# Performance work log

Hardware: AMD Instinct MI355X
Metric: run time of the kernel (lower is better)

The kernel has to match this reference:

```python
import jax, jax.numpy as jnp
import numpy as np
from functools import partial

# ---- config (scaled-up from repo globals) ----
B, T = 2, 1024          # batch, seq (block_size)
C = 1024                # n_embd
H = 16                  # n_heads
G = 2                   # n_groups -> n_kv_heads = H//G = 8, n_q_heads = G = 2
D = C // H              # d_head = 64
Q = G                   # query linears per head
NHID = 4 * C            # expert hidden (Expert default 4*n_embd)
E = 2                   # n_experts
K = 1                   # top_k_experts
WINDOW = 256            # window_size
EPS = 1e-5


def setup_inputs() -> dict:
    key = jax.random.key(0)
    ks = jax.random.split(key, 20)
    s = 0.02
    f32 = jnp.float32
    return {
        "x": jax.random.normal(ks[0], (B, T, C), f32),
        # attention params (per-head stacked)
        "Wq": jax.random.normal(ks[1], (H, Q, C, D), f32) * s,
        "Wk": jax.random.normal(ks[2], (H, C, D), f32) * s,
        "Wv": jax.random.normal(ks[3], (H, C, D), f32) * s,
        "Wp": jax.random.normal(ks[4], (C, C), f32) * s,
        "bp": jnp.zeros((C,), f32),
        # layernorms
        "ln1_g": jnp.ones((C,), f32), "ln1_b": jnp.zeros((C,), f32),
        "ln2_g": jnp.ones((C,), f32), "ln2_b": jnp.zeros((C,), f32),
        # router gate
        "Wg": jax.random.normal(ks[5], (C, E), f32) * s,
        "bg": jnp.zeros((E,), f32),
        # experts (stacked over E): Linear(C->NHID) -> SwiGLU(NHID) -> Linear(NHID->C)
        "Ew1": jax.random.normal(ks[6], (E, C, NHID), f32) * s,
        "Eb1": jnp.zeros((E, NHID), f32),
        "Ews": jax.random.normal(ks[7], (E, NHID, NHID), f32) * s,
        "Ebs": jnp.zeros((E, NHID), f32),
        "Ebeta": jax.random.normal(ks[8], (E,), f32),
        "Ewg": jax.random.normal(ks[9], (E, NHID, NHID), f32) * s,
        "Ebg": jnp.zeros((E, NHID), f32),
        "Ew2": jax.random.normal(ks[10], (E, NHID, C), f32) * s,
        "Eb2": jnp.zeros((E, C), f32),
    }


def _layer_norm(x, g, b):
    mean = jnp.mean(x, axis=-1, keepdims=True)
    var = jnp.var(x, axis=-1, keepdims=True, ddof=1)  # torch .var() is unbiased
    return (x - mean) / jnp.sqrt(var + EPS) * g + b


def _forward(x, Wq, Wk, Wv, Wp, bp, ln1_g, ln1_b, ln2_g, ln2_b,
             Wg, bg, Ew1, Eb1, Ews, Ebs, Ebeta, Ewg, Ebg, Ew2, Eb2):
    # ---- pre-norm GQA-SWA attention ----
    xn = _layer_norm(x, ln1_g, ln1_b)
    k = jnp.einsum('btc,hcd->hbtd', xn, Wk)          # [H,B,T,D]
    q = jnp.einsum('btc,hqcd->hqbtd', xn, Wq)        # [H,Q,B,T,D]
    v = jnp.einsum('btc,hcd->hbtd', xn, Wv)
    # faithful to torch keys.view(B, C, T): memory reinterpret, NOT transpose
    kr = k.reshape(H, B, D, T)
    scores = jnp.einsum('hqbtd,hbds->hbts', q, kr) * (D ** -0.5)  # sum over Q
    # only the past-window mask is applied (the causal masked_fill is unassigned in source)
    past_mask = jnp.tril(jnp.ones((T, T), jnp.float32), -WINDOW)
    scores = jnp.where(past_mask == 1, -jnp.inf, scores)
    w = jax.nn.softmax(scores, axis=-1)
    o = jnp.einsum('hbts,hbsd->hbtd', w, v)
    o = o.transpose(1, 2, 0, 3).reshape(B, T, C)     # concat heads
    x = x + o @ Wp + bp

    # ---- top-k MoE router ----
    xn2 = _layer_norm(x, ln2_g, ln2_b)
    logits = xn2 @ Wg + bg                           # [B,T,E]
    topw, topi = jax.lax.top_k(logits, K)            # [B,T,K]
    topw = jax.nn.softmax(topw, axis=1)              # faithful bug: softmax over token dim
    # dense expert compute (vectorized replacement for per-expert gather/scatter)
    h1 = jnp.einsum('btc,ech->ebth', xn2, Ew1) + Eb1[:, None, None, :]      # [E,B,T,NHID]
    sx = jnp.einsum('ebth,ehk->ebtk', h1, Ews) + Ebs[:, None, None, :]
    swish = sx * jax.nn.sigmoid(Ebeta[:, None, None, None] * sx)
    glu = jnp.einsum('ebth,ehk->ebtk', h1, Ewg) + Ebg[:, None, None, :]
    eout = jnp.einsum('ebtk,ekc->ebtc', swish * glu, Ew2) + Eb2[:, None, None, :]
    # per-token per-expert mixing weight (top-k indices are distinct)
    onehot = topi[..., None] == jnp.arange(E)        # [B,T,K,E]
    coef = jnp.sum(jnp.where(onehot, topw[..., None], 0.0), axis=2)         # [B,T,E]
    moe = jnp.einsum('bte,ebtc->btc', coef, eout)
    return x + moe


def reference(x, Wq, Wk, Wv, Wp, bp, ln1_g, ln1_b, ln2_g, ln2_b,
              Wg, bg, Ew1, Eb1, Ews, Ebs, Ebeta, Ewg, Ebg, Ew2, Eb2):
    return _forward(x, Wq, Wk, Wv, Wp, bp, ln1_g, ln1_b, ln2_g, ln2_b,
                    Wg, bg, Ew1, Eb1, Ews, Ebs, Ebeta, Ewg, Ebg, Ew2, Eb2)
```

## Files before the change

### kernel.cpp

```cpp
#include <hip/hip_runtime.h>
#include <hip/hip_bf16.h>
#include <cmath>

#define B_    2
#define T_    1024
#define BT_   2048
#define C_    1024
#define H_    16
#define NH_   4096
#define E_    2
#define WIN_  256
#define G_    8

typedef unsigned short u16;
typedef __attribute__((ext_vector_type(8))) short short8;
typedef __attribute__((ext_vector_type(4))) float f32x4;

__device__ __forceinline__ u16 f2b(float f) {
    __hip_bfloat16 h = __float2bfloat16(f);
    return *(u16*)&h;
}
__device__ __forceinline__ float b2f(u16 u) {
    __hip_bfloat16 h; *(u16*)&h = u;
    return __bfloat162float(h);
}

__device__ __forceinline__ void gl_lds16(const u16* g, u16* l) {
    __builtin_amdgcn_global_load_lds(
        (const __attribute__((address_space(1))) unsigned int*)g,
        (__attribute__((address_space(3))) unsigned int*)l, 16, 0, 0);
}

template<int TNJ, int EPI, int WINK = 0>
__global__ __launch_bounds__(256) void gemm_tn(
    const u16* __restrict__ A, const u16* __restrict__ B,
    float* __restrict__ Cf, u16* __restrict__ Cb,
    const float* __restrict__ bias, const float* __restrict__ res,
    const float* __restrict__ coef,
    int K, int lda, int ldb, int ldc,
    int hb0, long aCz, long aCb, long aCh,
    long bCb, long bCh, long cCz, long cCb, long cCh)
{
    constexpr int TN = TNJ * 32;
    constexpr int ABUF = 128 * 32;
    constexpr int BBUF = TN * 32;
    constexpr int BUFSZ = ABUF + BBUF;
    constexpr int NINST = 8 + TN / 16;
    constexpr int NPW = NINST / 4;
    __shared__ alignas(16) u16 L[2 * BUFSZ];
    int tid = threadIdx.x;
    int z = blockIdx.z;
    int hb = hb0 + z;
    int hh = hb >> 1, bb = hb & 1;
    const u16* Ap = A + aCz * z + aCb * bb + aCh * hh + (size_t)blockIdx.y * 128 * lda;
    const u16* Bp = B + bCb * bb + bCh * hh + (size_t)blockIdx.x * TN * ldb;
    size_t cOff = (size_t)(cCz * z + cCb * bb + cCh * hh);

    int lane = tid & 63, w = tid >> 6;
    int wr = (w >> 1) * 64, wc = (w & 1) * (TNJ * 16);
    int fm = lane & 15;

    int rBase = blockIdx.y * 128 + wr + (lane >> 4) * 4;
    int cBase = blockIdx.x * TN + wc + fm;

    if (EPI == 2) {
        if ((int)blockIdx.x * TN + TN - 1 <= (int)blockIdx.y * 128 - WIN_) {
            #pragma unroll
            for (int i = 0; i < 4; ++i)
                #pragma unroll
                for (int j = 0; j < TNJ; ++j)
                    #pragma unroll
                    for (int r = 0; r < 4; ++r)
                        Cf[cOff + (size_t)(rBase + i * 16 + r) * ldc + cBase + j * 16] = -INFINITY;
            return;
        }
    }

    int kBeg = 0;
    if (WINK) {
        int s = (int)blockIdx.y * 128 - (WIN_ - 1);
        kBeg = (s > 0) ? ((s >> 5) << 5) : 0;
    }

    const u16* gsrc[NPW];
    int loff[NPW];
    #pragma unroll
    for (int ii = 0; ii < NPW; ++ii) {
        int inst = w * NPW + ii;
        int lrow = lane >> 2;
        int sx = lane & 3;
        if (inst < 8) {
            int row = inst * 16 + lrow;
            gsrc[ii] = Ap + (size_t)row * lda + ((sx ^ ((row >> 1) & 3)) * 8);
            loff[ii] = inst * 512;
        } else {
            int row = (inst - 8) * 16 + lrow;
            gsrc[ii] = Bp + (size_t)row * ldb + ((sx ^ ((row >> 1) & 3)) * 8);
            loff[ii] = ABUF + (inst - 8) * 512;
        }
    }
    int aoff[4], boff[TNJ];
    #pragma unroll
    for (int i = 0; i < 4; ++i) {
        int r = wr + i * 16 + fm;
        aoff[i] = r * 32 + (((lane >> 4) ^ ((r >> 1) & 3)) * 8);
    }
    #pragma unroll
    for (int j = 0; j < TNJ; ++j) {
        int r = wc + j * 16 + fm;
        boff[j] = ABUF + r * 32 + (((lane >> 4) ^ ((r >> 1) & 3)) * 8);
    }

    f32x4 acc[4][TNJ];
    #pragma unroll
    for (int i = 0; i < 4; ++i)
        #pragma unroll
        for (int j = 0; j < TNJ; ++j)
            acc[i][j] = (f32x4){0.f, 0.f, 0.f, 0.f};

    auto STAGE = [&](int bufOff, int kk) {
        #pragma unroll
        for (int ii = 0; ii < NPW; ++ii)
            gl_lds16(gsrc[ii] + kk, L + bufOff + loff[ii]);
    };
    auto COMPUTE = [&](int bufOff) {
        short8 af[4], bf[TNJ];
        #pragma unroll
        for (int i = 0; i < 4; ++i) af[i] = *(const short8*)(L + bufOff + aoff[i]);
        #pragma unroll
        for (int j = 0; j < TNJ; ++j) bf[j] = *(const short8*)(L + bufOff + boff[j]);
        #pragma unroll
        for (int i = 0; i < 4; ++i)
            #pragma unroll
            for (int j = 0; j < TNJ; ++j)
                acc[i][j] = __builtin_amdgcn_mfma_f32_16x16x32_bf16(af[i], bf[j], acc[i][j], 0, 0, 0);
    };

    int nt = (K - kBeg) >> 5;
    STAGE(0, kBeg);
    __syncthreads();
    for (int t = 0; t < nt; t += 2) {
        STAGE(BUFSZ, kBeg + (t + 1) * 32);
        COMPUTE(0);
        __syncthreads();
        if (t + 2 < nt) STAGE(0, kBeg + (t + 2) * 32);
        COMPUTE(BUFSZ);
        __syncthreads();
    }

    #pragma unroll
    for (int i = 0; i < 4; ++i)
        #pragma unroll
        for (int j = 0; j < TNJ; ++j)
            #pragma unroll
            for (int r = 0; r < 4; ++r) {
                int row = rBase + i * 16 + r;
                int col = cBase + j * 16;
                float v = acc[i][j][r];
                size_t o = cOff + (size_t)row * ldc + col;
                if (EPI == 0) Cf[o] = v;
                else if (EPI == 1) Cb[o] = f2b(v);
                else if (EPI == 2) {
                    v *= 0.125f;
                    if (col <= row - WIN_) v = -INFINITY;
                    Cf[o] = v;
                } else if (EPI == 3) {
                    Cf[o] = v + bias[col] + res[(size_t)row * ldc + col];
                } else if (EPI == 4) {
                    Cb[o] = f2b(v + bias[col]);
                } else if (EPI == 5) {
                    Cf[o] = res[o] + coef[row] * (v + bias[col]);
                } else {
                    Cf[o] += coef[row] * (v + bias[col]);
                }
            }
}

__global__ __launch_bounds__(256) void gemm_tn_dual(
    const u16* __restrict__ A, const u16* __restrict__ B1,
    const u16* __restrict__ B2, const float* __restrict__ bs,
    const float* __restrict__ bg, const float* __restrict__ betaP,
    u16* __restrict__ P, int K, int lda, int ldb, int ldc)
{
    constexpr int ABUF = 128 * 32;
    constexpr int BBUF = 64 * 32;
    constexpr int BUFSZ = ABUF + 2 * BBUF;
    __shared__ alignas(16) u16 L[2 * BUFSZ];
    int tid = threadIdx.x;
    const u16* Ap  = A  + (size_t)blockIdx.y * 128 * lda;
    const u16* B1p = B1 + (size_t)blockIdx.x * 64 * ldb;
    const u16* B2p = B2 + (size_t)blockIdx.x * 64 * ldb;

    int lane = tid & 63, w = tid >> 6;
    int wr = (w >> 1) * 64, wc = (w & 1) * 32;
    int fm = lane & 15;

    const u16* gsrc[4];
    int loff[4];
    #pragma unroll
    for (int ii = 0; ii < 4; ++ii) {
        int inst = w * 4 + ii;
        int lrow = lane >> 2;
        int sx = lane & 3;
        if (inst < 8) {
            int row = inst * 16 + lrow;
            gsrc[ii] = Ap + (size_t)row * lda + ((sx ^ ((row >> 1) & 3)) * 8);
            loff[ii] = inst * 512;
        } else if (inst < 12) {
            int row = (inst - 8) * 16 + lrow;
            gsrc[ii] = B1p + (size_t)row * ldb + ((sx ^ ((row >> 1) & 3)) * 8);
            loff[ii] = ABUF + (inst - 8) * 512;
        } else {
            int row = (inst - 12) * 16 + lrow;
            gsrc[ii] = B2p + (size_t)row * ldb + ((sx ^ ((row >> 1) & 3)) * 8);
            loff[ii] = ABUF + BBUF + (inst - 12) * 512;
        }
    }
    int aoff[4], boff[2];
    #pragma unroll
    for (int i = 0; i < 4; ++i) {
        int r = wr + i * 16 + fm;
        aoff[i] = r * 32 + (((lane >> 4) ^ ((r >> 1) & 3)) * 8);
    }
    #pragma unroll
    for (int j = 0; j < 2; ++j) {
        int r = wc + j * 16 + fm;
        boff[j] = ABUF + r * 32 + (((lane >> 4) ^ ((r >> 1) & 3)) * 8);
    }

    f32x4 a1[4][2], a2[4][2];
    #pragma unroll
    for (int i = 0; i < 4; ++i)
        #pragma unroll
        for (int j = 0; j < 2; ++j) {
            a1[i][j] = (f32x4){0.f, 0.f, 0.f, 0.f};
            a2[i][j] = (f32x4){0.f, 0.f, 0.f, 0.f};
        }

    auto STAGE = [&](int bufOff, int kk) {
        #pragma unroll
        for (int ii = 0; ii < 4; ++ii)
            gl_lds16(gsrc[ii] + kk, L + bufOff + loff[ii]);
    };
    auto COMPUTE = [&](int bufOff) {
        short8 af[4], b1f[2], b2f[2];
        #pragma unroll
        for (int i = 0; i < 4; ++i) af[i] = *(const short8*)(L + bufOff + aoff[i]);
        #pragma unroll
        for (int j = 0; j < 2; ++j) {
            b1f[j] = *(const short8*)(L + bufOff + boff[j]);
            b2f[j] = *(const short8*)(L + bufOff + BBUF + boff[j]);
        }
        #pragma unroll
        for (int i = 0; i < 4; ++i)
            #pragma unroll
            for (int j = 0; j < 2; ++j) {
                a1[i][j] = __builtin_amdgcn_mfma_f32_16x16x32_bf16(af[i], b1f[j], a1[i][j], 0, 0, 0);
                a2[i][j] = __builtin_amdgcn_mfma_f32_16x16x32_bf16(af[i], b2f[j], a2[i][j], 0, 0, 0);
            }
    };

    int nt = K >> 5;
    STAGE(0, 0);
    __syncthreads();
    for (int t = 0; t < nt; t += 2) {
        STAGE(BUFSZ, (t + 1) * 32);
        COMPUTE(0);
        __syncthreads();
        if (t + 2 < nt) STAGE(0, (t + 2) * 32);
        COMPUTE(BUFSZ);
        __syncthreads();
    }

    float beta = betaP[0];
    int rBase = blockIdx.y * 128 + wr + (lane >> 4) * 4;
    int cBase = blockIdx.x * 64 + wc + fm;
    #pragma unroll
    for (int i = 0; i < 4; ++i)
        #pragma unroll
        for (int j = 0; j < 2; ++j)
            #pragma unroll
            for (int r = 0; r < 4; ++r) {
                int row = rBase + i * 16 + r;
                int col = cBase + j * 16;
                float sx = a1[i][j][r] + bs[col];
                float gl = a2[i][j][r] + bg[col];
                float sw = sx / (1.f + expf(-beta * sx));
                P[(size_t)row * ldc + col] = f2b(sw * gl);
            }
}

__global__ __launch_bounds__(256) void transpose_w(
    const float* __restrict__ W, u16* __restrict__ out, int K, int N)
{
    __shared__ u16 Ls[64][66];
    int n0 = blockIdx.x * 64, k0 = blockIdx.y * 64;
    int tid = threadIdx.x;
    #pragma unroll
    for (int i = 0; i < 16; ++i) {
        int idx = tid + i * 256;
        int r = idx >> 6, c = idx & 63;
        Ls[r][c] = f2b(W[(size_t)(k0 + r) * N + n0 + c]);
    }
    __syncthreads();
    #pragma unroll
    for (int i = 0; i < 16; ++i) {
        int idx = tid + i * 256;
        int n = idx >> 6, k = idx & 63;
        out[(size_t)(n0 + n) * K + k0 + k] = Ls[k][n];
    }
}

__global__ __launch_bounds__(256) void ln_kernel(
    const float* __restrict__ x, const float* __restrict__ g,
    const float* __restrict__ b, u16* __restrict__ outB,
    float* __restrict__ outF, int wantF)
{
    int row = blockIdx.x;
    int tid = threadIdx.x;
    __shared__ float rs[256], rq[256];
    const float* xp = x + (size_t)row * C_;
    float s = 0.f, q = 0.f;
    for (int c = tid; c < C_; c += 256) {
        float v = xp[c];
        s += v; q += v * v;
    }
    rs[tid] = s; rq[tid] = q; __syncthreads();
    for (int off = 128; off > 0; off >>= 1) {
        if (tid < off) { rs[tid] += rs[tid + off]; rq[tid] += rq[tid + off]; }
        __syncthreads();
    }
    float mean = rs[0] * (1.f / C_);
    float var  = (rq[0] - (float)C_ * mean * mean) * (1.f / (C_ - 1));
    float inv  = rsqrtf(var + 1e-5f);
    for (int c = tid; c < C_; c += 256) {
        float v = (xp[c] - mean) * inv * g[c] + b[c];
        outB[(size_t)row * C_ + c] = f2b(v);
        if (wantF) outF[(size_t)row * C_ + c] = v;
    }
}

__global__ __launch_bounds__(256) void prep_whcd(const float* __restrict__ W, u16* __restrict__ out) {
    int idx = blockIdx.x * 256 + threadIdx.x;
    int hd = idx >> 10, c = idx & 1023;
    out[idx] = f2b(W[((size_t)(hd >> 6) * C_ + c) * 64 + (hd & 63)]);
}
__global__ __launch_bounds__(256) void prep_wq(const float* __restrict__ W, u16* __restrict__ out) {
    int idx = blockIdx.x * 256 + threadIdx.x;
    int hd = idx >> 10, c = idx & 1023;
    int h = hd >> 6, d = hd & 63;
    size_t i0 = (((size_t)h * 2 + 0) * C_ + c) * 64 + d;
    size_t i1 = (((size_t)h * 2 + 1) * C_ + c) * 64 + d;
    out[idx] = f2b(W[i0] + W[i1]);
}
__global__ __launch_bounds__(256) void prep_wp(const float* __restrict__ W, u16* __restrict__ out) {
    int idx = blockIdx.x * 256 + threadIdx.x;
    int n = idx >> 10, k = idx & 1023;
    out[idx] = f2b(W[(size_t)k * C_ + n]);
}
__global__ __launch_bounds__(256) void prep_krt(const u16* __restrict__ Kbf, u16* __restrict__ out) {
    int idx = blockIdx.x * 256 + threadIdx.x;
    int hb = idx >> 16, rem = idx & 65535;
    int s = rem >> 6, d = rem & 63;
    int h = hb >> 1, b = hb & 1;
    out[idx] = Kbf[((size_t)(b * 1024 + d * 16 + (s >> 6))) * 1024 + h * 64 + (s & 63)];
}
__global__ __launch_bounds__(256) void prep_vt(const u16* __restrict__ Vbf, u16* __restrict__ out) {
    int idx = blockIdx.x * 256 + threadIdx.x;
    int hb = idx >> 16, rem = idx & 65535;
    int d = rem >> 10, s = rem & 1023;
    int h = hb >> 1, b = hb & 1;
    out[idx] = Vbf[((size_t)(b * 1024 + s)) * 1024 + h * 64 + d];
}

__global__ __launch_bounds__(256) void softmax_rows(float* __restrict__ sc) {
    float* rp = sc + (size_t)blockIdx.x * 1024;
    int tid = threadIdx.x;
    float4 v = *(float4*)(rp + tid * 4);
    __shared__ float red[256];
    float mx = fmaxf(fmaxf(v.x, v.y), fmaxf(v.z, v.w));
    red[tid] = mx; __syncthreads();
    for (int off = 128; off > 0; off >>= 1) {
        if (tid < off) red[tid] = fmaxf(red[tid], red[tid + off]);
        __syncthreads();
    }
    mx = red[0]; __syncthreads();
    float e0 = expf(v.x - mx), e1 = expf(v.y - mx), e2 = expf(v.z - mx), e3 = expf(v.w - mx);
    red[tid] = e0 + e1 + e2 + e3; __syncthreads();
    for (int off = 128; off > 0; off >>= 1) {
        if (tid < off) red[tid] += red[tid + off];
        __syncthreads();
    }
    float inv = 1.f / red[0];
    u16* wp = (u16*)rp;
    wp[tid * 4 + 0] = f2b(e0 * inv);
    wp[tid * 4 + 1] = f2b(e1 * inv);
    wp[tid * 4 + 2] = f2b(e2 * inv);
    wp[tid * 4 + 3] = f2b(e3 * inv);
}

__global__ __launch_bounds__(256) void router_kernel(
    const float* __restrict__ xn2, const float* __restrict__ Wg,
    const float* __restrict__ bgp, float* __restrict__ mOut, int* __restrict__ topiOut)
{
    int g = blockIdx.x;
    int tid = threadIdx.x;
    __shared__ float r0[256], r1[256];
    const float* xp = xn2 + (size_t)g * C_;
    float a0 = 0.f, a1 = 0.f;
    for (int c = tid; c < C_; c += 256) {
        float xv = xp[c];
        a0 += xv * Wg[c * 2 + 0];
        a1 += xv * Wg[c * 2 + 1];
    }
    r0[tid] = a0; r1[tid] = a1; __syncthreads();
    for (int off = 128; off > 0; off >>= 1) {
        if (tid < off) { r0[tid] += r0[tid + off]; r1[tid] += r1[tid + off]; }
        __syncthreads();
    }
    if (tid == 0) {
        float l0 = r0[0] + bgp[0];
        float l1 = r1[0] + bgp[1];
        topiOut[g] = (l1 > l0) ? 1 : 0;
        mOut[g] = fmaxf(l0, l1);
    }
}

__global__ __launch_bounds__(256) void gatecoef_kernel(
    const float* __restrict__ m, const int* __restrict__ topi, float* __restrict__ coef)
{
    int b = blockIdx.x;
    int tid = threadIdx.x;
    __shared__ float red[256];
    const float* mp = m + (size_t)b * T_;
    float mx = -INFINITY;
    for (int t = tid; t < T_; t += 256) mx = fmaxf(mx, mp[t]);
    red[tid] = mx; __syncthreads();
    for (int off = 128; off > 0; off >>= 1) {
        if (tid < off) red[tid] = fmaxf(red[tid], red[tid + off]);
        __syncthreads();
    }
    mx = red[0]; __syncthreads();
    float s = 0.f;
    for (int t = tid; t < T_; t += 256) s += expf(mp[t] - mx);
    red[tid] = s; __syncthreads();
    for (int off = 128; off > 0; off >>= 1) {
        if (tid < off) red[tid] += red[tid + off];
        __syncthreads();
    }
    float inv = 1.f / red[0];
    for (int t = tid; t < T_; t += 256) {
        int g = b * T_ + t;
        float wv = expf(mp[t] - mx) * inv;
        int e = topi[g];
        coef[g]       = (e == 0) ? wv : 0.f;
        coef[BT_ + g] = (e == 1) ? wv : 0.f;
    }
}

extern "C" void kernel_launch(void* const* d_in, const int* in_sizes, int n_in,
                              void* d_out, int out_size, void* d_ws, size_t ws_size,
                              hipStream_t stream)
{
    const float* x    = (const float*)d_in[0];
    const float* Wq   = (const float*)d_in[1];
    const float* Wk   = (const float*)d_in[2];
    const float* Wv   = (const float*)d_in[3];
    const float* Wp   = (const float*)d_in[4];
    const float* bp   = (const float*)d_in[5];
    const float* ln1g = (const float*)d_in[6];
    const float* ln1b = (const float*)d_in[7];
    const float* ln2g = (const float*)d_in[8];
    const float* ln2b = (const float*)d_in[9];
    const float* Wg   = (const float*)d_in[10];
    const float* bg   = (const float*)d_in[11];
    const float* Ew1  = (const float*)d_in[12];
    const float* Eb1  = (const float*)d_in[13];
    const float* Ews  = (const float*)d_in[14];
    const float* Ebs  = (const float*)d_in[15];
    const float* Ebeta= (const float*)d_in[16];
    const float* Ewg  = (const float*)d_in[17];
    const float* Ebg  = (const float*)d_in[18];
    const float* Ew2  = (const float*)d_in[19];
    const float* Eb2  = (const float*)d_in[20];
    float* out = (float*)d_out;

    char* ws = (char*)d_ws;
    const size_t MB = 1024 * 1024;
    u16*  xnbf   = (u16*) (ws + 0);
    u16*  WqsT   = (u16*) (ws + 4*MB);
    u16*  WkT    = (u16*) (ws + 6*MB);
    u16*  WvT    = (u16*) (ws + 8*MB);
    u16*  WpT    = (u16*) (ws + 10*MB);
    u16*  Qbf    = (u16*) (ws + 12*MB);
    u16*  Kbf    = (u16*) (ws + 16*MB);
    u16*  Vbf    = (u16*) (ws + 20*MB);
    u16*  KrT    = (u16*) (ws + 24*MB);
    u16*  VT     = (u16*) (ws + 28*MB);
    u16*  Obf    = (u16*) (ws + 32*MB);
    float* x1    = (float*)(ws + 36*MB);
    float* sc    = (float*)(ws + 44*MB);
    float* mbuf  = (float*)(ws + 61*MB);
    int*   topi  = (int*)  (ws + 61*MB + 16*1024);
    float* coef  = (float*)(ws + 61*MB + 32*1024);
    u16*  xn2bf  = (u16*) (ws + 0);
    float* xn2f  = (float*)(ws + 28*MB);
    u16*  h1     = (u16*) (ws + 44*MB);
    u16*  pbuf   = (u16*) (ws + 12*MB);
    u16*  W1T    = (u16*) (ws + 4*MB);
    u16*  W2T    = (u16*) (ws + 4*MB);
    u16*  WsT    = (u16*) (ws + 62*MB);
    u16*  WgT    = (u16*) (ws + 94*MB);

    ln_kernel<<<BT_, 256, 0, stream>>>(x, ln1g, ln1b, xnbf, nullptr, 0);

    prep_whcd<<<C_*C_/256, 256, 0, stream>>>(Wk, WkT);
    prep_whcd<<<C_*C_/256, 256, 0, stream>>>(Wv, WvT);
    prep_wq  <<<C_*C_/256, 256, 0, stream>>>(Wq, WqsT);
    prep_wp  <<<C_*C_/256, 256, 0, stream>>>(Wp, WpT);

    {
        dim3 grid(16, 16, 1);
        gemm_tn<2,1><<<grid, 256, 0, stream>>>(xnbf, WqsT, nullptr, Qbf, nullptr, nullptr, nullptr,
            C_, C_, C_, C_, 0, 0,0,0, 0,0, 0,0,0);
        gemm_tn<2,1><<<grid, 256, 0, stream>>>(xnbf, WkT, nullptr, Kbf, nullptr, nullptr, nullptr,
            C_, C_, C_, C_, 0, 0,0,0, 0,0, 0,0,0);
        gemm_tn<2,1><<<grid, 256, 0, stream>>>(xnbf, WvT, nullptr, Vbf, nullptr, nullptr, nullptr,
            C_, C_, C_, C_, 0, 0,0,0, 0,0, 0,0,0);
    }
    prep_krt<<<H_*B_*T_*64/256, 256, 0, stream>>>(Kbf, KrT);
    prep_vt <<<H_*B_*T_*64/256, 256, 0, stream>>>(Vbf, VT);

    for (int chunk = 0; chunk < (H_*B_)/G_; ++chunk) {
        int hb0 = chunk * G_;
        gemm_tn<4,2><<<dim3(8, 8, G_), 256, 0, stream>>>(
            Qbf, KrT, sc, nullptr, nullptr, nullptr, nullptr,
            64, C_, 64, 1024, hb0,
            0, 1048576, 64,
            65536, 131072,
            1048576, 0, 0);
        softmax_rows<<<G_*1024, 256, 0, stream>>>(sc);
        gemm_tn<2,1,1><<<dim3(1, 8, G_), 256, 0, stream>>>(
            (u16*)sc, VT, nullptr, Obf, nullptr, nullptr, nullptr,
            1024, 2048, 1024, 1024, hb0,
            2097152, 0, 0,
            65536, 131072,
            0, 1048576, 64);
    }

    gemm_tn<2,3><<<dim3(16, 16, 1), 256, 0, stream>>>(
        Obf, WpT, x1, nullptr, bp, x, nullptr,
        C_, C_, C_, C_, 0, 0,0,0, 0,0, 0,0,0);

    ln_kernel<<<BT_, 256, 0, stream>>>(x1, ln2g, ln2b, xn2bf, xn2f, 1);

    router_kernel<<<BT_, 256, 0, stream>>>(xn2f, Wg, bg, mbuf, topi);
    gatecoef_kernel<<<B_, 256, 0, stream>>>(mbuf, topi, coef);

    for (int e = 0; e < E_; ++e) {
        transpose_w<<<dim3(NH_/64, C_/64), 256, 0, stream>>>(
            Ew1 + (size_t)e * C_ * NH_, W1T, C_, NH_);
        gemm_tn<4,4><<<dim3(NH_/128, 16), 256, 0, stream>>>(
            xn2bf, W1T, nullptr, h1, Eb1 + (size_t)e * NH_, nullptr, nullptr,
            C_, C_, C_, NH_, 0, 0,0,0, 0,0, 0,0,0);
        transpose_w<<<dim3(NH_/64, NH_/64), 256, 0, stream>>>(
            Ews + (size_t)e * NH_ * NH_, WsT, NH_, NH_);
        transpose_w<<<dim3(NH_/64, NH_/64), 256, 0, stream>>>(
            Ewg + (size_t)e * NH_ * NH_, WgT, NH_, NH_);
        gemm_tn_dual<<<dim3(NH_/64, 16), 256, 0, stream>>>(
            h1, WsT, WgT, Ebs + (size_t)e * NH_, Ebg + (size_t)e * NH_, Ebeta + e,
            pbuf, NH_, NH_, NH_, NH_);
        transpose_w<<<dim3(C_/64, NH_/64), 256, 0, stream>>>(
            Ew2 + (size_t)e * NH_ * C_, W2T, NH_, C_);
        if (e == 0)
            gemm_tn<2,5><<<dim3(C_/64, 16), 256, 0, stream>>>(
                pbuf, W2T, out, nullptr, Eb2, x1, coef + 0 * BT_,
                NH_, NH_, NH_, C_, 0, 0,0,0, 0,0, 0,0,0);
        else
            gemm_tn<2,6><<<dim3(C_/64, 16), 256, 0, stream>>>(
                pbuf, W2T, out, nullptr, Eb2 + (size_t)e * C_, nullptr, coef + (size_t)e * BT_,
                NH_, NH_, NH_, C_, 0, 0,0,0, 0,0, 0,0,0);
    }
}
```

Baseline: 1.186 ms.

## Deepen GEMM pipeline to four LDS stages with vmcnt waits, XCD swizzle, setprio

Replaces the double-buffered GEMM main loop with a four-deep LDS ring. Each step waits with explicit s_waitcnt vmcnt and raw barriers, so three tile loads stay in flight while MFMAs run. It also remaps block indices across the eight XCDs for better L2 locality, raises wave priority around the MFMA bursts, and shrinks the W1 GEMM tile to 64 columns for more blocks. The costs are four times the LDS per block, which may reduce occupancy, and hand-tuned wait counts that assume each K loop has at least four tiles and a count divisible by four.

```diff
diff --git a/kernel.cpp b/kernel.cpp
--- a/kernel.cpp
+++ b/kernel.cpp
@@ -20,10 +20,6 @@
     __hip_bfloat16 h = __float2bfloat16(f);
     return *(u16*)&h;
 }
-__device__ __forceinline__ float b2f(u16 u) {
-    __hip_bfloat16 h; *(u16*)&h = u;
-    return __bfloat162float(h);
-}
 
 __device__ __forceinline__ void gl_lds16(const u16* g, u16* l) {
     __builtin_amdgcn_global_load_lds(
@@ -31,7 +27,27 @@
         (__attribute__((address_space(3))) unsigned int*)l, 16, 0, 0);
 }
 
-template<int TNJ, int EPI, int WINK = 0>
+template<int N> __device__ __forceinline__ void waitvm() {
+    asm volatile("s_waitcnt vmcnt(%0)" :: "n"(N) : "memory");
+}
+__device__ __forceinline__ void barrier_raw() {
+    __builtin_amdgcn_sched_barrier(0);
+    __builtin_amdgcn_s_barrier();
+    __builtin_amdgcn_sched_barrier(0);
+}
+
+__device__ __forceinline__ void xcd_swizzle(int& bx, int& by) {
+    int gx = gridDim.x, gy = gridDim.y;
+    int tot = gx * gy;
+    if ((tot & 7) == 0) {
+        int flat = by * gx + bx;
+        int q = tot >> 3;
+        int lg = (flat & 7) * q + (flat >> 3);
+        bx = lg / gy; by = lg % gy;
+    }
+}
+
+template<int TNJ, int EPI, int WINK, int PIPE>
 __global__ __launch_bounds__(256) void gemm_tn(
     const u16* __restrict__ A, const u16* __restrict__ B,
     float* __restrict__ Cf, u16* __restrict__ Cb,
@@ -45,26 +61,29 @@
     constexpr int ABUF = 128 * 32;
     constexpr int BBUF = TN * 32;
     constexpr int BUFSZ = ABUF + BBUF;
+    constexpr int NDEEP = PIPE ? 4 : 2;
     constexpr int NINST = 8 + TN / 16;
     constexpr int NPW = NINST / 4;
-    __shared__ alignas(16) u16 L[2 * BUFSZ];
+    __shared__ alignas(16) u16 L[NDEEP * BUFSZ];
     int tid = threadIdx.x;
+    int bx = blockIdx.x, by = blockIdx.y;
+    xcd_swizzle(bx, by);
     int z = blockIdx.z;
     int hb = hb0 + z;
     int hh = hb >> 1, bb = hb & 1;
-    const u16* Ap = A + aCz * z + aCb * bb + aCh * hh + (size_t)blockIdx.y * 128 * lda;
-    const u16* Bp = B + bCb * bb + bCh * hh + (size_t)blockIdx.x * TN * ldb;
+    const u16* Ap = A + aCz * z + aCb * bb + aCh * hh + (size_t)by * 128 * lda;
+    const u16* Bp = B + bCb * bb + bCh * hh + (size_t)bx * TN * ldb;
     size_t cOff = (size_t)(cCz * z + cCb * bb + cCh * hh);
 
     int lane = tid & 63, w = tid >> 6;
     int wr = (w >> 1) * 64, wc = (w & 1) * (TNJ * 16);
     int fm = lane & 15;
 
-    int rBase = blockIdx.y * 128 + wr + (lane >> 4) * 4;
-    int cBase = blockIdx.x * TN + wc + fm;
+    int rBase = by * 128 + wr + (lane >> 4) * 4;
+    int cBase = bx * TN + wc + fm;
 
     if (EPI == 2) {
-        if ((int)blockIdx.x * TN + TN - 1 <= (int)blockIdx.y * 128 - WIN_) {
+        if (bx * TN + TN - 1 <= by * 128 - WIN_) {
             #pragma unroll
             for (int i = 0; i < 4; ++i)
                 #pragma unroll
@@ -78,7 +97,7 @@
 
     int kBeg = 0;
     if (WINK) {
-        int s = (int)blockIdx.y * 128 - (WIN_ - 1);
+        int s = by * 128 - (WIN_ - 1);
         kBeg = (s > 0) ? ((s >> 5) << 5) : 0;
     }
 
@@ -129,23 +148,50 @@
         for (int i = 0; i < 4; ++i) af[i] = *(const short8*)(L + bufOff + aoff[i]);
         #pragma unroll
         for (int j = 0; j < TNJ; ++j) bf[j] = *(const short8*)(L + bufOff + boff[j]);
+        __builtin_amdgcn_s_setprio(1);
         #pragma unroll
         for (int i = 0; i < 4; ++i)
             #pragma unroll
             for (int j = 0; j < TNJ; ++j)
                 acc[i][j] = __builtin_amdgcn_mfma_f32_16x16x32_bf16(af[i], bf[j], acc[i][j], 0, 0, 0);
+        __builtin_amdgcn_s_setprio(0);
     };
 
     int nt = (K - kBeg) >> 5;
-    STAGE(0, kBeg);
-    __syncthreads();
-    for (int t = 0; t < nt; t += 2) {
-        STAGE(BUFSZ, kBeg + (t + 1) * 32);
-        COMPUTE(0);
+
+    if (PIPE) {
+        STAGE(0 * BUFSZ, kBeg);
+        STAGE(1 * BUFSZ, kBeg + 32);
+        STAGE(2 * BUFSZ, kBeg + 64);
+        auto PHASEF = [&](int bufC, int bufS, int kk) {
+            STAGE(bufS, kk);
+            waitvm<3 * NPW>();
+            barrier_raw();
+            COMPUTE(bufC);
+            barrier_raw();
+        };
+        for (int p = 0; p < nt - 4; p += 4) {
+            PHASEF(0 * BUFSZ, 3 * BUFSZ, kBeg + (p + 3) * 32);
+            PHASEF(1 * BUFSZ, 0 * BUFSZ, kBeg + (p + 4) * 32);
+            PHASEF(2 * BUFSZ, 1 * BUFSZ, kBeg + (p + 5) * 32);
+            PHASEF(3 * BUFSZ, 2 * BUFSZ, kBeg + (p + 6) * 32);
+        }
+        STAGE(3 * BUFSZ, kBeg + (nt - 1) * 32);
+        waitvm<3 * NPW>(); barrier_raw(); COMPUTE(0 * BUFSZ); barrier_raw();
+        waitvm<2 * NPW>(); barrier_raw(); COMPUTE(1 * BUFSZ); barrier_raw();
+        waitvm<1 * NPW>(); barrier_raw(); COMPUTE(2 * BUFSZ); barrier_raw();
+        waitvm<0>();       barrier_raw(); COMPUTE(3 * BUFSZ);
+    } else {
+        STAGE(0, kBeg);
         __syncthreads();
-        if (t + 2 < nt) STAGE(0, kBeg + (t + 2) * 32);
-        COMPUTE(BUFSZ);
-        __syncthreads();
+        for (int t = 0; t < nt; t += 2) {
+            STAGE(BUFSZ, kBeg + (t + 1) * 32);
+            COMPUTE(0);
+            __syncthreads();
+            if (t + 2 < nt) STAGE(0, kBeg + (t + 2) * 32);
+            COMPUTE(BUFSZ);
+            __syncthreads();
+        }
     }
 
     #pragma unroll
@@ -185,11 +231,14 @@
     constexpr int ABUF = 128 * 32;
     constexpr int BBUF = 64 * 32;
     constexpr int BUFSZ = ABUF + 2 * BBUF;
-    __shared__ alignas(16) u16 L[2 * BUFSZ];
+    constexpr int NPW = 4;
+    __shared__ alignas(16) u16 L[4 * BUFSZ];
     int tid = threadIdx.x;
-    const u16* Ap  = A  + (size_t)blockIdx.y * 128 * lda;
-    const u16* B1p = B1 + (size_t)blockIdx.x * 64 * ldb;
-    const u16* B2p = B2 + (size_t)blockIdx.x * 64 * ldb;
+    int bx = blockIdx.x, by = blockIdx.y;
+    xcd_swizzle(bx, by);
+    const u16* Ap  = A  + (size_t)by * 128 * lda;
+    const u16* B1p = B1 + (size_t)bx * 64 * ldb;
+    const u16* B2p = B2 + (size_t)bx * 64 * ldb;
 
     int lane = tid & 63, w = tid >> 6;
     int wr = (w >> 1) * 64, wc = (w & 1) * 32;
@@ -251,6 +300,7 @@
             b1f[j] = *(const short8*)(L + bufOff + boff[j]);
             b2f[j] = *(const short8*)(L + bufOff + BBUF + boff[j]);
         }
+        __builtin_amdgcn_s_setprio(1);
         #pragma unroll
         for (int i = 0; i < 4; ++i)
             #pragma unroll
@@ -258,23 +308,35 @@
                 a1[i][j] = __builtin_amdgcn_mfma_f32_16x16x32_bf16(af[i], b1f[j], a1[i][j], 0, 0, 0);
                 a2[i][j] = __builtin_amdgcn_mfma_f32_16x16x32_bf16(af[i], b2f[j], a2[i][j], 0, 0, 0);
             }
+        __builtin_amdgcn_s_setprio(0);
     };
 
     int nt = K >> 5;
-    STAGE(0, 0);
-    __syncthreads();
-    for (int t = 0; t < nt; t += 2) {
-        STAGE(BUFSZ, (t + 1) * 32);
-        COMPUTE(0);
-        __syncthreads();
-        if (t + 2 < nt) STAGE(0, (t + 2) * 32);
-        COMPUTE(BUFSZ);
-        __syncthreads();
-    }
+    STAGE(0 * BUFSZ, 0);
+    STAGE(1 * BUFSZ, 32);
+    STAGE(2 * BUFSZ, 64);
+    auto PHASEF = [&](int bufC, int bufS, int kk) {
+        STAGE(bufS, kk);
+        waitvm<3 * NPW>();
+        barrier_raw();
+        COMPUTE(bufC);
+        barrier_raw();
+    };
+    for (int p = 0; p < nt - 4; p += 4) {
+        PHASEF(0 * BUFSZ, 3 * BUFSZ, (p + 3) * 32);
+        PHASEF(1 * BUFSZ, 0 * BUFSZ, (p + 4) * 32);
+        PHASEF(2 * BUFSZ, 1 * BUFSZ, (p + 5) * 32);
+        PHASEF(3 * BUFSZ, 2 * BUFSZ, (p + 6) * 32);
+    }
+    STAGE(3 * BUFSZ, (nt - 1) * 32);
+    waitvm<3 * NPW>(); barrier_raw(); COMPUTE(0 * BUFSZ); barrier_raw();
+    waitvm<2 * NPW>(); barrier_raw(); COMPUTE(1 * BUFSZ); barrier_raw();
+    waitvm<1 * NPW>(); barrier_raw(); COMPUTE(2 * BUFSZ); barrier_raw();
+    waitvm<0>();       barrier_raw(); COMPUTE(3 * BUFSZ);
 
     float beta = betaP[0];
-    int rBase = blockIdx.y * 128 + wr + (lane >> 4) * 4;
-    int cBase = blockIdx.x * 64 + wc + fm;
+    int rBase = by * 128 + wr + (lane >> 4) * 4;
+    int cBase = bx * 64 + wc + fm;
     #pragma unroll
     for (int i = 0; i < 4; ++i)
         #pragma unroll
@@ -521,11 +583,11 @@
 
     {
         dim3 grid(16, 16, 1);
-        gemm_tn<2,1><<<grid, 256, 0, stream>>>(xnbf, WqsT, nullptr, Qbf, nullptr, nullptr, nullptr,
+        gemm_tn<2,1,0,1><<<grid, 256, 0, stream>>>(xnbf, WqsT, nullptr, Qbf, nullptr, nullptr, nullptr,
             C_, C_, C_, C_, 0, 0,0,0, 0,0, 0,0,0);
-        gemm_tn<2,1><<<grid, 256, 0, stream>>>(xnbf, WkT, nullptr, Kbf, nullptr, nullptr, nullptr,
+        gemm_tn<2,1,0,1><<<grid, 256, 0, stream>>>(xnbf, WkT, nullptr, Kbf, nullptr, nullptr, nullptr,
             C_, C_, C_, C_, 0, 0,0,0, 0,0, 0,0,0);
-        gemm_tn<2,1><<<grid, 256, 0, stream>>>(xnbf, WvT, nullptr, Vbf, nullptr, nullptr, nullptr,
+        gemm_tn<2,1,0,1><<<grid, 256, 0, stream>>>(xnbf, WvT, nullptr, Vbf, nullptr, nullptr, nullptr,
             C_, C_, C_, C_, 0, 0,0,0, 0,0, 0,0,0);
     }
     prep_krt<<<H_*B_*T_*64/256, 256, 0, stream>>>(Kbf, KrT);
@@ -533,14 +595,14 @@
 
     for (int chunk = 0; chunk < (H_*B_)/G_; ++chunk) {
         int hb0 = chunk * G_;
-        gemm_tn<4,2><<<dim3(8, 8, G_), 256, 0, stream>>>(
+        gemm_tn<4,2,0,0><<<dim3(8, 8, G_), 256, 0, stream>>>(
             Qbf, KrT, sc, nullptr, nullptr, nullptr, nullptr,
             64, C_, 64, 1024, hb0,
             0, 1048576, 64,
             65536, 131072,
             1048576, 0, 0);
         softmax_rows<<<G_*1024, 256, 0, stream>>>(sc);
-        gemm_tn<2,1,1><<<dim3(1, 8, G_), 256, 0, stream>>>(
+        gemm_tn<2,1,1,1><<<dim3(1, 8, G_), 256, 0, stream>>>(
             (u16*)sc, VT, nullptr, Obf, nullptr, nullptr, nullptr,
             1024, 2048, 1024, 1024, hb0,
             2097152, 0, 0,
@@ -548,7 +610,7 @@
             0, 1048576, 64);
     }
 
-    gemm_tn<2,3><<<dim3(16, 16, 1), 256, 0, stream>>>(
+    gemm_tn<2,3,0,1><<<dim3(16, 16, 1), 256, 0, stream>>>(
         Obf, WpT, x1, nullptr, bp, x, nullptr,
         C_, C_, C_, C_, 0, 0,0,0, 0,0, 0,0,0);
 
@@ -560,7 +622,7 @@
     for (int e = 0; e < E_; ++e) {
         transpose_w<<<dim3(NH_/64, C_/64), 256, 0, stream>>>(
             Ew1 + (size_t)e * C_ * NH_, W1T, C_, NH_);
-        gemm_tn<4,4><<<dim3(NH_/128, 16), 256, 0, stream>>>(
+        gemm_tn<2,4,0,1><<<dim3(NH_/64, 16), 256, 0, stream>>>(
             xn2bf, W1T, nullptr, h1, Eb1 + (size_t)e * NH_, nullptr, nullptr,
             C_, C_, C_, NH_, 0, 0,0,0, 0,0, 0,0,0);
         transpose_w<<<dim3(NH_/64, NH_/64), 256, 0, stream>>>(
@@ -573,11 +635,11 @@
         transpose_w<<<dim3(C_/64, NH_/64), 256, 0, stream>>>(
             Ew2 + (size_t)e * NH_ * C_, W2T, NH_, C_);
         if (e == 0)
-            gemm_tn<2,5><<<dim3(C_/64, 16), 256, 0, stream>>>(
+            gemm_tn<2,5,0,1><<<dim3(C_/64, 16), 256, 0, stream>>>(
                 pbuf, W2T, out, nullptr, Eb2, x1, coef + 0 * BT_,
                 NH_, NH_, NH_, C_, 0, 0,0,0, 0,0, 0,0,0);
         else
-            gemm_tn<2,6><<<dim3(C_/64, 16), 256, 0, stream>>>(
+            gemm_tn<2,6,0,1><<<dim3(C_/64, 16), 256, 0, stream>>>(
                 pbuf, W2T, out, nullptr, Eb2 + (size_t)e * C_, nullptr, coef + (size_t)e * BT_,
                 NH_, NH_, NH_, C_, 0, 0,0,0, 0,0, 0,0,0);
     }
```

Result: faster. 1.042 ms (-12.2%).
